# Kernel tuning notes

Hardware: AMD Instinct MI355X
Metric: run time of the kernel (lower is better)

Reference implementation:

```python
import jax, jax.numpy as jnp
import numpy as np

L, H, D, DH, F, V, S, B, CTX = 6, 12, 768, 64, 3072, 32000, 1024, 2, 1024
EPS = 1e-5


def layernorm(x, scale, bias):
    mu = jnp.mean(x, axis=-1, keepdims=True)
    var = jnp.mean(jnp.square(x - mu), axis=-1, keepdims=True)
    return (x - mu) * jax.lax.rsqrt(var + EPS) * scale + bias


def setup_inputs() -> dict:
    key = jax.random.key(0)
    ks = jax.random.split(key, 16)
    std = 0.02
    res_std = 0.02 * (2 * L) ** (-0.5)
    inp = {
        "X": jax.random.randint(ks[0], (B, S), 0, V),
        "emb": jax.random.normal(ks[1], (V, D), jnp.float32) * std,            # tied with head weight
        "pos_emb": jax.random.normal(ks[2], (CTX, D), jnp.float32) * 0.01,
        "Wq": jax.random.normal(ks[3], (L, H, D, DH), jnp.float32) * std,
        "bq": jnp.zeros((L, H, DH), jnp.float32),
        "Wk": jax.random.normal(ks[4], (L, H, D, DH), jnp.float32) * std,
        "bk": jnp.zeros((L, H, DH), jnp.float32),
        "Wv": jax.random.normal(ks[5], (L, H, D, DH), jnp.float32) * std,
        "bv": jnp.zeros((L, H, DH), jnp.float32),
        "Wo": jax.random.normal(ks[6], (L, H * DH, D), jnp.float32) * res_std,  # ResidualScaledLinear
        "bo": jnp.zeros((L, D), jnp.float32),
        "ln1_s": jnp.ones((L, D), jnp.float32),
        "ln1_b": jnp.zeros((L, D), jnp.float32),
        "ln2_s": jnp.ones((L, D), jnp.float32),
        "ln2_b": jnp.zeros((L, D), jnp.float32),
        "W1": jax.random.normal(ks[7], (L, D, F), jnp.float32) * std,
        "b1": jnp.zeros((L, F), jnp.float32),
        "W2": jax.random.normal(ks[8], (L, F, D), jnp.float32) * res_std,       # ResidualScaledLinear
        "b2": jnp.zeros((L, D), jnp.float32),
        "lnf_s": jnp.ones((D,), jnp.float32),
        "lnf_b": jnp.zeros((D,), jnp.float32),
        "head_b": jnp.zeros((V,), jnp.float32),
    }
    return inp


def decoder_forward(X, emb, pos_emb, Wq, bq, Wk, bk, Wv, bv, Wo, bo,
                    ln1_s, ln1_b, ln2_s, ln2_b, W1, b1, W2, b2,
                    lnf_s, lnf_b, head_b):
    seq = X.shape[1]
    x = emb[X] + pos_emb[:seq]                      # [B,S,D]
    causal = jnp.tril(jnp.ones((seq, seq), bool))   # tril mask buffer
    scale = 1.0 / jnp.sqrt(jnp.float32(DH))
    for l in range(L):
        xn = layernorm(x, ln1_s[l], ln1_b[l])
        q = jnp.einsum('bsd,hdk->bhsk', xn, Wq[l]) + bq[l][None, :, None, :]
        k = jnp.einsum('bsd,hdk->bhsk', xn, Wk[l]) + bk[l][None, :, None, :]
        v = jnp.einsum('bsd,hdk->bhsk', xn, Wv[l]) + bv[l][None, :, None, :]
        scores = jnp.einsum('bhsk,bhtk->bhst', q, k) * scale
        scores = jnp.where(causal, scores, -jnp.inf)
        attn = jax.nn.softmax(scores, axis=-1)
        out = jnp.einsum('bhst,bhtk->bshk', attn, v).reshape(x.shape[0], seq, H * DH)
        x = x + out @ Wo[l] + bo[l]
        xn2 = layernorm(x, ln2_s[l], ln2_b[l])
        x = x + jax.nn.relu(xn2 @ W1[l] + b1[l]) @ W2[l] + b2[l]
    x = layernorm(x, lnf_s, lnf_b)
    return x @ emb.T + head_b                       # tied head weight


def reference(X, emb, pos_emb, Wq, bq, Wk, bk, Wv, bv, Wo, bo,
              ln1_s, ln1_b, ln2_s, ln2_b, W1, b1, W2, b2,
              lnf_s, lnf_b, head_b):
    return decoder_forward(X, emb, pos_emb, Wq, bq, Wk, bk, Wv, bv, Wo, bo,
                           ln1_s, ln1_b, ln2_s, ln2_b, W1, b1, W2, b2,
                           lnf_s, lnf_b, head_b)
```

## Files before the change

kernel.cpp:

```cpp
#include <hip/hip_runtime.h>
#include <cstdint>
#include <cstddef>

#define CL 6
#define CH 12
#define CD 768
#define CDH 64
#define CF 3072
#define CV 32000
#define CS 1024
#define CB 2
#define CM (CB*CS)
#define CQS 2304
#define PSTRIDE 4224

typedef unsigned short u16;
typedef __bf16 bf16x8 __attribute__((ext_vector_type(8)));
typedef float f32x4 __attribute__((ext_vector_type(4)));

__device__ __forceinline__ float bf2f(u16 u) {
  union { unsigned int i; float f; } c; c.i = ((unsigned int)u) << 16; return c.f;
}
__device__ __forceinline__ u16 f2bf(float f) {
  union { float f; unsigned int i; } c; c.f = f;
  unsigned int lsb = (c.i >> 16) & 1u;
  c.i += 0x7fffu + lsb;
  return (u16)(c.i >> 16);
}

__device__ __forceinline__ void gload16(const u16* g, u16* l) {
  __builtin_amdgcn_global_load_lds(
      (const __attribute__((address_space(1))) void*)g,
      (__attribute__((address_space(3))) void*)l, 16, 0, 0);
}

__global__ __launch_bounds__(256) void convert_kernel(
    const float* __restrict__ src, u16* __restrict__ dst, int total)
{
  int idx = blockIdx.x * 256 + threadIdx.x;
  if (idx < total) dst[idx] = f2bf(src[idx]);
}

__global__ __launch_bounds__(256) void embed_kernel(
    const int* __restrict__ X, const float* __restrict__ emb,
    const float* __restrict__ pos, float* __restrict__ x)
{
  int idx = blockIdx.x * 256 + threadIdx.x;
  int m = idx / CD, d = idx - m * CD;
  int s = m & (CS - 1);
  x[idx] = emb[(size_t)X[m] * CD + d] + pos[s * CD + d];
}

__global__ __launch_bounds__(256) void ln_kernel(
    const float* __restrict__ x, const float* __restrict__ gs,
    const float* __restrict__ gb, u16* __restrict__ out)
{
  __shared__ float rs[4], rss[4];
  int row = blockIdx.x, tid = threadIdx.x;
  const float* xr = x + (size_t)row * CD;
  float a0 = xr[tid], a1 = xr[tid + 256], a2 = xr[tid + 512];
  float s = a0 + a1 + a2;
  float ss = a0 * a0 + a1 * a1 + a2 * a2;
#pragma unroll
  for (int sh = 32; sh > 0; sh >>= 1) {
    s  += __shfl_xor(s, sh, 64);
    ss += __shfl_xor(ss, sh, 64);
  }
  int w = tid >> 6;
  if ((tid & 63) == 0) { rs[w] = s; rss[w] = ss; }
  __syncthreads();
  s  = rs[0] + rs[1] + rs[2] + rs[3];
  ss = rss[0] + rss[1] + rss[2] + rss[3];
  float mu = s * (1.f / CD);
  float inv = rsqrtf(ss * (1.f / CD) - mu * mu + 1e-5f);
  u16* orow = out + (size_t)row * CD;
  orow[tid]       = f2bf((a0 - mu) * inv * gs[tid]       + gb[tid]);
  orow[tid + 256] = f2bf((a1 - mu) * inv * gs[tid + 256] + gb[tid + 256]);
  orow[tid + 512] = f2bf((a2 - mu) * inv * gs[tid + 512] + gb[tid + 512]);
}

__global__ __launch_bounds__(256) void trans_kernel(
    u16* __restrict__ dst, const float* __restrict__ src, int R, int C,
    int PB, long dstL)
{
  __shared__ float st[32][65];
  int r0 = blockIdx.x * 64, c0 = blockIdx.y * 32, bz = blockIdx.z;
  const float* s = src + (size_t)bz * R * C;
  u16* d = dst + (size_t)(bz / PB) * dstL + (size_t)(bz % PB) * R * C;
  int tx = threadIdx.x & 31, ty = threadIdx.x >> 5;
#pragma unroll
  for (int i = 0; i < 8; i++) {
    int r = ty + 8 * i;
    st[tx][r] = s[(size_t)(r0 + r) * C + c0 + tx];
  }
  __syncthreads();
  int j = threadIdx.x & 15, cbase = threadIdx.x >> 4;
#pragma unroll
  for (int i = 0; i < 2; i++) {
    int c = cbase + 16 * i;
    uint2 pk;
    u16* p = (u16*)&pk;
    p[0] = f2bf(st[c][4 * j + 0]);
    p[1] = f2bf(st[c][4 * j + 1]);
    p[2] = f2bf(st[c][4 * j + 2]);
    p[3] = f2bf(st[c][4 * j + 3]);
    *(uint2*)&d[(size_t)(c0 + c) * R + r0 + 4 * j] = pk;
  }
}

__global__ __launch_bounds__(256) void biaspack_kernel(
    const float* __restrict__ bq, const float* __restrict__ bk,
    const float* __restrict__ bv, float* __restrict__ dst)
{
  int idx = blockIdx.x * 256 + threadIdx.x;
  int l = idx / CQS, c = idx - l * CQS;
  float val;
  if (c < 768)       val = bq[l * 768 + c];
  else if (c < 1536) val = bk[l * 768 + c - 768];
  else               val = bv[l * 768 + c - 1536];
  dst[idx] = val;
}

template<bool RES, bool RELU, bool OUTBF>
__global__ __launch_bounds__(256) void gemm64v3_kernel(
    const u16* __restrict__ A, const u16* __restrict__ Bt,
    const float* __restrict__ bias, const float* __restrict__ res,
    void* __restrict__ outp, int M, int N, int K)
{
  __shared__ __align__(16) u16 As[64 * 32];
  __shared__ __align__(16) u16 Bs[64 * 32];
  int tid = threadIdx.x;
  int m0 = blockIdx.y * 64, n0 = blockIdx.x * 64;
  int wv = tid >> 6, ln = tid & 63;
  int quad = ln >> 4, l16 = ln & 15;
  int wm = (wv >> 1) * 32, wn = (wv & 1) * 32;
  int srow = tid >> 2, scol = (tid & 3) * 8;
  const u16* gA = A  + (size_t)(m0 + srow) * K + scol;
  const u16* gB = Bt + (size_t)(n0 + srow) * K + scol;
  u16* lA = As + wv * 512;
  u16* lB = Bs + wv * 512;

  f32x4 acc[2][2];
  acc[0][0] = f32x4{0,0,0,0}; acc[0][1] = f32x4{0,0,0,0};
  acc[1][0] = f32x4{0,0,0,0}; acc[1][1] = f32x4{0,0,0,0};

  for (int kt = 0; kt < K; kt += 32) {
    __syncthreads();
    gload16(gA + kt, lA);
    gload16(gB + kt, lB);
    __syncthreads();
    bf16x8 af[2], bfr[2];
#pragma unroll
    for (int i = 0; i < 2; i++) {
      af[i]  = *reinterpret_cast<const bf16x8*>(&As[(wm + i * 16 + l16) * 32 + quad * 8]);
      bfr[i] = *reinterpret_cast<const bf16x8*>(&Bs[(wn + i * 16 + l16) * 32 + quad * 8]);
    }
#pragma unroll
    for (int i = 0; i < 2; i++)
#pragma unroll
      for (int j = 0; j < 2; j++)
        acc[i][j] = __builtin_amdgcn_mfma_f32_16x16x32_bf16(af[i], bfr[j], acc[i][j], 0, 0, 0);
  }

#pragma unroll
  for (int i = 0; i < 2; i++) {
    int gmb = m0 + wm + i * 16 + quad * 4;
#pragma unroll
    for (int j = 0; j < 2; j++) {
      int gn = n0 + wn + j * 16 + l16;
      float bsv = bias[gn];
#pragma unroll
      for (int rr = 0; rr < 4; rr++) {
        float val = acc[i][j][rr] + bsv;
        if (RELU) val = fmaxf(val, 0.f);
        size_t o = (size_t)(gmb + rr) * N + gn;
        if (RES) val += res[o];
        if (OUTBF) ((u16*)outp)[o] = f2bf(val);
        else       ((float*)outp)[o] = val;
      }
    }
  }
}

template<bool RES, bool RELU, bool OUTBF>
__global__ __launch_bounds__(256) void gemm128_kernel(
    const u16* __restrict__ A, const u16* __restrict__ Bt,
    const float* __restrict__ bias, const float* __restrict__ res,
    void* __restrict__ outp, int M, int N, int K)
{
  __shared__ __align__(16) u16 As[128 * 32];
  __shared__ __align__(16) u16 Bs[128 * 32];
  int tid = threadIdx.x;
  int nbm = M >> 7, nbn = N >> 7, nwg = nbm * nbn;
  int orig = blockIdx.x;
  int q8 = nwg >> 3, r8 = nwg & 7;
  int xcd = orig & 7;
  int t = ((xcd < r8) ? xcd * (q8 + 1) : r8 * (q8 + 1) + (xcd - r8) * q8) + (orig >> 3);
  int bm = t % nbm, bn = t / nbm;
  int m0 = bm << 7, n0 = bn << 7;

  int wv = tid >> 6, ln = tid & 63;
  int quad = ln >> 4, l16 = ln & 15;
  int wr = wv >> 1, wc = wv & 1;

  int srow = wv * 16 + (ln >> 2);
  int scol = (ln & 3) * 8;
  const u16* ga0 = A  + (size_t)(m0 + srow) * K + scol;
  const u16* ga1 = A  + (size_t)(m0 + srow + 64) * K + scol;
  const u16* gb0 = Bt + (size_t)(n0 + srow) * K + scol;
  const u16* gb1 = Bt + (size_t)(n0 + srow + 64) * K + scol;
  u16* lA0 = As + wv * 512;
  u16* lA1 = As + 2048 + wv * 512;
  u16* lB0 = Bs + wv * 512;
  u16* lB1 = Bs + 2048 + wv * 512;

  f32x4 acc[4][4];
#pragma unroll
  for (int i = 0; i < 4; i++)
#pragma unroll
    for (int j = 0; j < 4; j++) acc[i][j] = f32x4{0.f, 0.f, 0.f, 0.f};

  for (int kt = 0; kt < K; kt += 32) {
    __syncthreads();
    gload16(ga0 + kt, lA0);
    gload16(ga1 + kt, lA1);
    gload16(gb0 + kt, lB0);
    gload16(gb1 + kt, lB1);
    __syncthreads();
    bf16x8 af[4], bf[4];
#pragma unroll
    for (int i = 0; i < 4; i++)
      af[i] = *reinterpret_cast<const bf16x8*>(&As[(wr * 64 + i * 16 + l16) * 32 + quad * 8]);
#pragma unroll
    for (int j = 0; j < 4; j++)
      bf[j] = *reinterpret_cast<const bf16x8*>(&Bs[(wc * 64 + j * 16 + l16) * 32 + quad * 8]);
#pragma unroll
    for (int i = 0; i < 4; i++)
#pragma unroll
      for (int j = 0; j < 4; j++)
        acc[i][j] = __builtin_amdgcn_mfma_f32_16x16x32_bf16(af[i], bf[j], acc[i][j], 0, 0, 0);
  }

#pragma unroll
  for (int i = 0; i < 4; i++) {
    int gm = m0 + wr * 64 + i * 16 + quad * 4;
#pragma unroll
    for (int j = 0; j < 4; j++) {
      int gn = n0 + wc * 64 + j * 16 + l16;
      float bsv = bias[gn];
#pragma unroll
      for (int rr = 0; rr < 4; rr++) {
        float val = acc[i][j][rr] + bsv;
        if (RELU) val = fmaxf(val, 0.f);
        size_t oo = (size_t)(gm + rr) * N + gn;
        if (RES) val += res[oo];
        if (OUTBF) ((u16*)outp)[oo] = f2bf(val);
        else       ((float*)outp)[oo] = val;
      }
    }
  }
}

__global__ __launch_bounds__(256) void attn_mfma_kernel(
    const u16* __restrict__ qkv, u16* __restrict__ o, float* __restrict__ part)
{
  __shared__ __align__(16) u16 Ks[2][64 * 64];
  __shared__ __align__(16) u16 Vt[2][64 * 64];
  __shared__ __align__(16) u16 Ps[4 * 16 * 64];

  int tid = threadIdx.x;
  int a = blockIdx.x;
  int h = blockIdx.y, b = blockIdx.z;
  int wid = tid >> 6, lane = tid & 63, quad = lane >> 4, l16 = lane & 15;

  int qb, ts, te, chunk;
  if (a < 16) {
    qb = 15 - (a >> 1);
    int half = (qb + 1) >> 1;
    if (a & 1) { ts = 0; te = half - 1; chunk = 0; }
    else       { ts = half; te = qb;    chunk = 1; }
  } else { qb = 23 - a; ts = 0; te = qb; chunk = -1; }

  int q0 = qb * 64;
  size_t bh = (size_t)b * CS * CQS + h * CDH;

  const u16* kbase = qkv + bh + 768;
  const u16* vbase = qkv + bh + 1536;

  int t4 = (tid & 15) * 4, dg = (tid >> 4) * 4;

  bf16x8 aq[2];
  {
    const u16* qrow = qkv + bh + (size_t)(q0 + wid * 16 + l16) * CQS;
#pragma unroll
    for (int ks = 0; ks < 2; ks++) {
      uint4 t = *(const uint4*)(qrow + ks * 32 + quad * 8);
      aq[ks] = *reinterpret_cast<bf16x8*>(&t);
    }
  }

  f32x4 oacc[4];
  float mrow[4], lrow[4];
#pragma unroll
  for (int j = 0; j < 4; j++) oacc[j] = f32x4{0.f, 0.f, 0.f, 0.f};
#pragma unroll
  for (int r = 0; r < 4; r++) { mrow[r] = -1e30f; lrow[r] = 0.f; }

  {
    const u16* kb0 = kbase + (size_t)ts * 64 * CQS;
#pragma unroll
    for (int it = 0; it < 2; it++) {
      int c = it * 256 + tid;
      int row = c >> 3, c8l = c & 7;
      gload16(kb0 + (size_t)row * CQS + (((c8l ^ (row & 7)) * 8)),
              &Ks[0][(it * 256 + wid * 64) * 8]);
    }
    const u16* vb0 = vbase + (size_t)ts * 64 * CQS;
    uint2 vr[4];
#pragma unroll
    for (int i = 0; i < 4; i++)
      vr[i] = *(const uint2*)(vb0 + (size_t)(t4 + i) * CQS + dg);
#pragma unroll
    for (int j = 0; j < 4; j++) {
      int d = dg + j;
      uint2 pk;
      u16* p = (u16*)&pk;
      p[0] = ((const u16*)&vr[0])[j]; p[1] = ((const u16*)&vr[1])[j];
      p[2] = ((const u16*)&vr[2])[j]; p[3] = ((const u16*)&vr[3])[j];
      *(uint2*)&Vt[0][d * 64 + (((t4 >> 3) ^ (d & 7)) * 8) + (t4 & 4)] = pk;
    }
  }

  for (int tt = ts; tt <= te; tt++) {
    int t0 = tt * 64;
    int cur = (tt - ts) & 1;
    __syncthreads();
    bool hasnext = (tt < te);
    uint2 vr[4];
    if (hasnext) {
      const u16* vb2 = vbase + (size_t)(t0 + 64) * CQS;
#pragma unroll
      for (int i = 0; i < 4; i++)
        vr[i] = *(const uint2*)(vb2 + (size_t)(t4 + i) * CQS + dg);
      const u16* kb2 = kbase + (size_t)(t0 + 64) * CQS;
#pragma unroll
      for (int it = 0; it < 2; it++) {
        int c = it * 256 + tid;
        int row = c >> 3, c8l = c & 7;
        gload16(kb2 + (size_t)row * CQS + (((c8l ^ (row & 7)) * 8)),
                &Ks[cur ^ 1][(it * 256 + wid * 64) * 8]);
      }
    }

    f32x4 sacc[4];
#pragma unroll
    for (int j = 0; j < 4; j++) sacc[j] = f32x4{0.f, 0.f, 0.f, 0.f};
#pragma unroll
    for (int j = 0; j < 4; j++) {
      int row = j * 16 + l16;
#pragma unroll
      for (int ks = 0; ks < 2; ks++) {
        bf16x8 bk = *reinterpret_cast<const bf16x8*>(
            &Ks[cur][row * 64 + ((((ks * 4 + quad) ^ (row & 7)) * 8))]);
        sacc[j] = __builtin_amdgcn_mfma_f32_16x16x32_bf16(aq[ks], bk, sacc[j], 0, 0, 0);
      }
    }

    int qg0 = q0 + wid * 16 + quad * 4;
#pragma unroll
    for (int j = 0; j < 4; j++) {
      int tg = t0 + j * 16 + l16;
#pragma unroll
      for (int r = 0; r < 4; r++) {
        float s = sacc[j][r] * 0.125f;
        sacc[j][r] = (tg <= qg0 + r) ? s : -1e30f;
      }
    }

#pragma unroll
    for (int r = 0; r < 4; r++) {
      float m = fmaxf(fmaxf(sacc[0][r], sacc[1][r]), fmaxf(sacc[2][r], sacc[3][r]));
#pragma unroll
      for (int sh = 1; sh < 16; sh <<= 1) m = fmaxf(m, __shfl_xor(m, sh, 64));
      float mnew = fmaxf(mrow[r], m);
      float scal = __expf(mrow[r] - mnew);
      mrow[r] = mnew;
      lrow[r] *= scal;
#pragma unroll
      for (int j = 0; j < 4; j++) oacc[j][r] *= scal;
      float sum = 0.f;
#pragma unroll
      for (int j = 0; j < 4; j++) {
        float p = __expf(sacc[j][r] - mnew);
        sacc[j][r] = p;
        sum += p;
      }
#pragma unroll
      for (int sh = 1; sh < 16; sh <<= 1) sum += __shfl_xor(sum, sh, 64);
      lrow[r] += sum;
    }

    u16* Pw = Ps + wid * 1024;
#pragma unroll
    for (int j = 0; j < 4; j++) {
      int c = (l16 >> 3) + 2 * j;
#pragma unroll
      for (int r = 0; r < 4; r++) {
        int row = quad * 4 + r;
        Pw[row * 64 + (((c ^ (row & 7)) * 8) | (l16 & 7))] = f2bf(sacc[j][r]);
      }
    }

    bf16x8 ap[2];
#pragma unroll
    for (int ks = 0; ks < 2; ks++)
      ap[ks] = *reinterpret_cast<const bf16x8*>(
          &Pw[l16 * 64 + ((((ks * 4 + quad) ^ (l16 & 7)) * 8))]);
#pragma unroll
    for (int j = 0; j < 4; j++) {
      int row = j * 16 + l16;
#pragma unroll
      for (int ks = 0; ks < 2; ks++) {
        bf16x8 bv = *reinterpret_cast<const bf16x8*>(
            &Vt[cur][row * 64 + ((((ks * 4 + quad) ^ (row & 7)) * 8))]);
        oacc[j] = __builtin_amdgcn_mfma_f32_16x16x32_bf16(ap[ks], bv, oacc[j], 0, 0, 0);
      }
    }

    if (hasnext) {
#pragma unroll
      for (int j = 0; j < 4; j++) {
        int d = dg + j;
        uint2 pk;
        u16* p = (u16*)&pk;
        p[0] = ((const u16*)&vr[0])[j]; p[1] = ((const u16*)&vr[1])[j];
        p[2] = ((const u16*)&vr[2])[j]; p[3] = ((const u16*)&vr[3])[j];
        *(uint2*)&Vt[cur ^ 1][d * 64 + (((t4 >> 3) ^ (d & 7)) * 8) + (t4 & 4)] = pk;
      }
    }
  }

  if (chunk < 0) {
#pragma unroll
    for (int r = 0; r < 4; r++) {
      float inv = 1.f / lrow[r];
      int qg = q0 + wid * 16 + quad * 4 + r;
      u16* orow = o + (size_t)b * CS * CD + h * CDH + (size_t)qg * CD;
#pragma unroll
      for (int j = 0; j < 4; j++)
        orow[j * 16 + l16] = f2bf(oacc[j][r] * inv);
    }
  } else {
    float* Po = part + (size_t)(((b * CH + h) * 8 + (qb - 8)) * 2 + chunk) * PSTRIDE;
#pragma unroll
    for (int r = 0; r < 4; r++) {
      int row = wid * 16 + quad * 4 + r;
#pragma unroll
      for (int j = 0; j < 4; j++)
        Po[row * 64 + j * 16 + l16] = oacc[j][r];
      if (l16 == 0) { Po[4096 + row] = mrow[r]; Po[4160 + row] = lrow[r]; }
    }
  }
}

__global__ __launch_bounds__(256) void attn_combine_kernel(
    const float* __restrict__ part, u16* __restrict__ o)
{
  int qb = 8 + blockIdx.x, h = blockIdx.y, b = blockIdx.z;
  const float* P0 = part + (size_t)(((b * CH + h) * 8 + (qb - 8)) * 2) * PSTRIDE;
  const float* P1 = P0 + PSTRIDE;
  int t = threadIdx.x;
  int row = t >> 2, c0 = (t & 3) * 16;
  float m0 = P0[4096 + row], m1 = P1[4096 + row];
  float m = fmaxf(m0, m1);
  float w0 = __expf(m0 - m), w1 = __expf(m1 - m);
  float inv = 1.f / (P0[4160 + row] * w0 + P1[4160 + row] * w1);
  u16* orow = o + (size_t)b * CS * CD + h * CDH + (size_t)(qb * 64 + row) * CD;
#pragma unroll
  for (int j = 0; j < 16; j++) {
    int col = c0 + j;
    orow[col] = f2bf((P0[row * 64 + col] * w0 + P1[row * 64 + col] * w1) * inv);
  }
}

extern "C" void kernel_launch(void* const* d_in, const int* in_sizes, int n_in,
                              void* d_out, int out_size, void* d_ws, size_t ws_size,
                              hipStream_t stream) {
  const int*   X      = (const int*)d_in[0];
  const float* emb    = (const float*)d_in[1];
  const float* pos    = (const float*)d_in[2];
  const float* Wq     = (const float*)d_in[3];
  const float* bq     = (const float*)d_in[4];
  const float* Wk     = (const float*)d_in[5];
  const float* bk     = (const float*)d_in[6];
  const float* Wv     = (const float*)d_in[7];
  const float* bv     = (const float*)d_in[8];
  const float* Wo     = (const float*)d_in[9];
  const float* bo     = (const float*)d_in[10];
  const float* ln1s   = (const float*)d_in[11];
  const float* ln1b   = (const float*)d_in[12];
  const float* ln2s   = (const float*)d_in[13];
  const float* ln2b   = (const float*)d_in[14];
  const float* W1     = (const float*)d_in[15];
  const float* b1     = (const float*)d_in[16];
  const float* W2     = (const float*)d_in[17];
  const float* b2     = (const float*)d_in[18];
  const float* lnfs   = (const float*)d_in[19];
  const float* lnfb   = (const float*)d_in[20];
  const float* headb  = (const float*)d_in[21];
  (void)in_sizes; (void)n_in; (void)out_size;

  char* ws = (char*)d_ws;
  size_t off = 0;
  auto alloc = [&](size_t bytes) { void* p = ws + off; off += (bytes + 255) & ~(size_t)255; return p; };

  float* x     = (float*)alloc((size_t)CM * CD * 4);
  u16*   xn    = (u16*)  alloc((size_t)CM * CD * 2);
  u16*   qkvb  = (u16*)  alloc((size_t)CM * CQS * 2);
  u16*   ao    = (u16*)  alloc((size_t)CM * CD * 2);
  u16*   hb    = (u16*)  alloc((size_t)CM * CF * 2);
  u16*   embC  = (u16*)  alloc((size_t)CV * CD * 2);
  float* biasp = (float*)alloc((size_t)CL * CQS * 4);
  float* part  = (float*)alloc((size_t)CB * CH * 8 * 2 * PSTRIDE * 4);

  const size_t WQKV = (size_t)CQS * CD;
  const size_t WOO  = (size_t)CD * CD;
  const size_t WFF  = (size_t)CD * CF;
  size_t perLayerElems = WQKV + WOO + 2 * WFF;
  bool fused = (ws_size >= off + (size_t)CL * perLayerElems * 2 + 4096);
  int LW = fused ? CL : 1;
  u16* Wqkvt = (u16*)alloc((size_t)LW * WQKV * 2);
  u16* Wot   = (u16*)alloc((size_t)LW * WOO * 2);
  u16* W1t   = (u16*)alloc((size_t)LW * WFF * 2);
  u16* W2t   = (u16*)alloc((size_t)LW * WFF * 2);

  embed_kernel<<<CM * CD / 256, 256, 0, stream>>>(X, emb, pos, x);
  convert_kernel<<<(CV * CD) / 256, 256, 0, stream>>>(emb, embC, CV * CD);
  biaspack_kernel<<<(CL * CQS) / 256, 256, 0, stream>>>(bq, bk, bv, biasp);

  if (fused) {
    trans_kernel<<<dim3(CD / 64, CDH / 32, CL * CH), 256, 0, stream>>>(Wqkvt,              Wq, CD, CDH, CH, (long)WQKV);
    trans_kernel<<<dim3(CD / 64, CDH / 32, CL * CH), 256, 0, stream>>>(Wqkvt + 768 * 768,  Wk, CD, CDH, CH, (long)WQKV);
    trans_kernel<<<dim3(CD / 64, CDH / 32, CL * CH), 256, 0, stream>>>(Wqkvt + 1536 * 768, Wv, CD, CDH, CH, (long)WQKV);
    trans_kernel<<<dim3(CD / 64, CD / 32, CL), 256, 0, stream>>>(Wot, Wo, CD, CD, 1, (long)WOO);
    trans_kernel<<<dim3(CD / 64, CF / 32, CL), 256, 0, stream>>>(W1t, W1, CD, CF, 1, (long)WFF);
    trans_kernel<<<dim3(CF / 64, CD / 32, CL), 256, 0, stream>>>(W2t, W2, CF, CD, 1, (long)WFF);
  }

  const int QKV_TOT = CH * CD * CDH;

  for (int l = 0; l < CL; l++) {
    if (!fused) {
      trans_kernel<<<dim3(CD / 64, CDH / 32, CH), 256, 0, stream>>>(Wqkvt,              Wq + (size_t)l * QKV_TOT, CD, CDH, CH, (long)WQKV);
      trans_kernel<<<dim3(CD / 64, CDH / 32, CH), 256, 0, stream>>>(Wqkvt + 768 * 768,  Wk + (size_t)l * QKV_TOT, CD, CDH, CH, (long)WQKV);
      trans_kernel<<<dim3(CD / 64, CDH / 32, CH), 256, 0, stream>>>(Wqkvt + 1536 * 768, Wv + (size_t)l * QKV_TOT, CD, CDH, CH, (long)WQKV);
      trans_kernel<<<dim3(CD / 64, CD / 32, 1), 256, 0, stream>>>(Wot, Wo + (size_t)l * WOO, CD, CD, 1, (long)WOO);
      trans_kernel<<<dim3(CD / 64, CF / 32, 1), 256, 0, stream>>>(W1t, W1 + (size_t)l * WFF, CD, CF, 1, (long)WFF);
      trans_kernel<<<dim3(CF / 64, CD / 32, 1), 256, 0, stream>>>(W2t, W2 + (size_t)l * WFF, CF, CD, 1, (long)WFF);
    }
    int lw = fused ? l : 0;
    const u16* wqkv = Wqkvt + (size_t)lw * WQKV;
    const u16* wot  = Wot   + (size_t)lw * WOO;
    const u16* w1t  = W1t   + (size_t)lw * WFF;
    const u16* w2t  = W2t   + (size_t)lw * WFF;

    ln_kernel<<<CM, 256, 0, stream>>>(x, ln1s + l * CD, ln1b + l * CD, xn);

    gemm128_kernel<false, false, true><<<(CM / 128) * (CQS / 128), 256, 0, stream>>>(
        xn, wqkv, biasp + l * CQS, nullptr, qkvb, CM, CQS, CD);

    attn_mfma_kernel<<<dim3(24, CH, CB), 256, 0, stream>>>(qkvb, ao, part);
    attn_combine_kernel<<<dim3(8, CH, CB), 256, 0, stream>>>(part, ao);

    gemm64v3_kernel<true, false, false><<<dim3(CD / 64, CM / 64), 256, 0, stream>>>(
        ao, wot, bo + l * CD, x, x, CM, CD, CD);

    ln_kernel<<<CM, 256, 0, stream>>>(x, ln2s + l * CD, ln2b + l * CD, xn);

    gemm128_kernel<false, true, true><<<(CM / 128) * (CF / 128), 256, 0, stream>>>(
        xn, w1t, b1 + l * CF, nullptr, hb, CM, CF, CD);

    gemm64v3_kernel<true, false, false><<<dim3(CD / 64, CM / 64), 256, 0, stream>>>(
        hb, w2t, b2 + l * CD, x, x, CM, CD, CF);
  }

  ln_kernel<<<CM, 256, 0, stream>>>(x, lnfs, lnfb, xn);
  gemm128_kernel<false, false, false><<<(CM / 128) * (CV / 128), 256, 0, stream>>>(
      xn, embC, headb, nullptr, d_out, CM, CV, CD);
}
```

Baseline: 1.508 ms.

## Double-buffer GEMM tiles, add 256-tile head GEMM, lazy softmax rescale

Converts the 64- and 128-tile GEMM kernels to double-buffered shared memory, so the next K-slice is loaded while the current one runs on MFMA, with one barrier per iteration instead of two. Adds a new 256x256-tile, 512-thread GEMM with swizzled LDS for the large vocabulary head projection. In attention it raises wave priority around MFMA blocks and skips the online-softmax rescale unless the running max grows by more than a threshold. The lazy rescale trades exactness of the running max for fewer exp and multiply operations, and risks overflow if scores drift. Larger LDS use may lower occupancy.

```diff
diff --git a/kernel.cpp b/kernel.cpp
--- a/kernel.cpp
+++ b/kernel.cpp
@@ -127,8 +127,8 @@
     const float* __restrict__ bias, const float* __restrict__ res,
     void* __restrict__ outp, int M, int N, int K)
 {
-  __shared__ __align__(16) u16 As[64 * 32];
-  __shared__ __align__(16) u16 Bs[64 * 32];
+  __shared__ __align__(16) u16 As[2][64 * 32];
+  __shared__ __align__(16) u16 Bs[2][64 * 32];
   int tid = threadIdx.x;
   int m0 = blockIdx.y * 64, n0 = blockIdx.x * 64;
   int wv = tid >> 6, ln = tid & 63;
@@ -137,29 +137,33 @@
   int srow = tid >> 2, scol = (tid & 3) * 8;
   const u16* gA = A  + (size_t)(m0 + srow) * K + scol;
   const u16* gB = Bt + (size_t)(n0 + srow) * K + scol;
-  u16* lA = As + wv * 512;
-  u16* lB = Bs + wv * 512;
 
   f32x4 acc[2][2];
   acc[0][0] = f32x4{0,0,0,0}; acc[0][1] = f32x4{0,0,0,0};
   acc[1][0] = f32x4{0,0,0,0}; acc[1][1] = f32x4{0,0,0,0};
 
+  gload16(gA, &As[0][wv * 512]);
+  gload16(gB, &Bs[0][wv * 512]);
+  __syncthreads();
+  int cur = 0;
   for (int kt = 0; kt < K; kt += 32) {
-    __syncthreads();
-    gload16(gA + kt, lA);
-    gload16(gB + kt, lB);
-    __syncthreads();
+    if (kt + 32 < K) {
+      gload16(gA + kt + 32, &As[cur ^ 1][wv * 512]);
+      gload16(gB + kt + 32, &Bs[cur ^ 1][wv * 512]);
+    }
     bf16x8 af[2], bfr[2];
 #pragma unroll
     for (int i = 0; i < 2; i++) {
-      af[i]  = *reinterpret_cast<const bf16x8*>(&As[(wm + i * 16 + l16) * 32 + quad * 8]);
-      bfr[i] = *reinterpret_cast<const bf16x8*>(&Bs[(wn + i * 16 + l16) * 32 + quad * 8]);
+      af[i]  = *reinterpret_cast<const bf16x8*>(&As[cur][(wm + i * 16 + l16) * 32 + quad * 8]);
+      bfr[i] = *reinterpret_cast<const bf16x8*>(&Bs[cur][(wn + i * 16 + l16) * 32 + quad * 8]);
     }
 #pragma unroll
     for (int i = 0; i < 2; i++)
 #pragma unroll
       for (int j = 0; j < 2; j++)
         acc[i][j] = __builtin_amdgcn_mfma_f32_16x16x32_bf16(af[i], bfr[j], acc[i][j], 0, 0, 0);
+    __syncthreads();
+    cur ^= 1;
   }
 
 #pragma unroll
@@ -188,8 +192,8 @@
     const float* __restrict__ bias, const float* __restrict__ res,
     void* __restrict__ outp, int M, int N, int K)
 {
-  __shared__ __align__(16) u16 As[128 * 32];
-  __shared__ __align__(16) u16 Bs[128 * 32];
+  __shared__ __align__(16) u16 As[2][128 * 32];
+  __shared__ __align__(16) u16 Bs[2][128 * 32];
   int tid = threadIdx.x;
   int nbm = M >> 7, nbn = N >> 7, nwg = nbm * nbn;
   int orig = blockIdx.x;
@@ -209,10 +213,6 @@
   const u16* ga1 = A  + (size_t)(m0 + srow + 64) * K + scol;
   const u16* gb0 = Bt + (size_t)(n0 + srow) * K + scol;
   const u16* gb1 = Bt + (size_t)(n0 + srow + 64) * K + scol;
-  u16* lA0 = As + wv * 512;
-  u16* lA1 = As + 2048 + wv * 512;
-  u16* lB0 = Bs + wv * 512;
-  u16* lB1 = Bs + 2048 + wv * 512;
 
   f32x4 acc[4][4];
 #pragma unroll
@@ -220,25 +220,33 @@
 #pragma unroll
     for (int j = 0; j < 4; j++) acc[i][j] = f32x4{0.f, 0.f, 0.f, 0.f};
 
+  gload16(ga0, &As[0][wv * 512]);
+  gload16(ga1, &As[0][2048 + wv * 512]);
+  gload16(gb0, &Bs[0][wv * 512]);
+  gload16(gb1, &Bs[0][2048 + wv * 512]);
+  __syncthreads();
+  int cur = 0;
   for (int kt = 0; kt < K; kt += 32) {
-    __syncthreads();
-    gload16(ga0 + kt, lA0);
-    gload16(ga1 + kt, lA1);
-    gload16(gb0 + kt, lB0);
-    gload16(gb1 + kt, lB1);
-    __syncthreads();
+    if (kt + 32 < K) {
+      gload16(ga0 + kt + 32, &As[cur ^ 1][wv * 512]);
+      gload16(ga1 + kt + 32, &As[cur ^ 1][2048 + wv * 512]);
+      gload16(gb0 + kt + 32, &Bs[cur ^ 1][wv * 512]);
+      gload16(gb1 + kt + 32, &Bs[cur ^ 1][2048 + wv * 512]);
+    }
     bf16x8 af[4], bf[4];
 #pragma unroll
     for (int i = 0; i < 4; i++)
-      af[i] = *reinterpret_cast<const bf16x8*>(&As[(wr * 64 + i * 16 + l16) * 32 + quad * 8]);
+      af[i] = *reinterpret_cast<const bf16x8*>(&As[cur][(wr * 64 + i * 16 + l16) * 32 + quad * 8]);
 #pragma unroll
     for (int j = 0; j < 4; j++)
-      bf[j] = *reinterpret_cast<const bf16x8*>(&Bs[(wc * 64 + j * 16 + l16) * 32 + quad * 8]);
+      bf[j] = *reinterpret_cast<const bf16x8*>(&Bs[cur][(wc * 64 + j * 16 + l16) * 32 + quad * 8]);
 #pragma unroll
     for (int i = 0; i < 4; i++)
 #pragma unroll
       for (int j = 0; j < 4; j++)
         acc[i][j] = __builtin_amdgcn_mfma_f32_16x16x32_bf16(af[i], bf[j], acc[i][j], 0, 0, 0);
+    __syncthreads();
+    cur ^= 1;
   }
 
 #pragma unroll
@@ -254,6 +262,98 @@
         if (RELU) val = fmaxf(val, 0.f);
         size_t oo = (size_t)(gm + rr) * N + gn;
         if (RES) val += res[oo];
+        if (OUTBF) ((u16*)outp)[oo] = f2bf(val);
+        else       ((float*)outp)[oo] = val;
+      }
+    }
+  }
+}
+
+template<bool OUTBF>
+__global__ __launch_bounds__(512, 2) void gemm256_kernel(
+    const u16* __restrict__ A, const u16* __restrict__ Bt,
+    const float* __restrict__ bias, void* __restrict__ outp,
+    int M, int N, int K)
+{
+  __shared__ __align__(16) u16 As[2][256 * 64];
+  __shared__ __align__(16) u16 Bs[2][256 * 64];
+  int tid = threadIdx.x;
+  int nbm = M >> 8, nbn = N >> 8, nwg = nbm * nbn;
+  int orig = blockIdx.x;
+  int q8 = nwg >> 3, r8 = nwg & 7;
+  int xcd = orig & 7;
+  int t = ((xcd < r8) ? xcd * (q8 + 1) : r8 * (q8 + 1) + (xcd - r8) * q8) + (orig >> 3);
+  int bm = t % nbm, bn = t / nbm;
+  int m0 = bm << 8, n0 = bn << 8;
+
+  int wv = tid >> 6, ln = tid & 63;
+  int quad = ln >> 4, l16 = ln & 15;
+  int wr = wv >> 2, wc = wv & 3;
+
+  int srow = tid >> 3;
+  int scol = (((tid & 7) ^ (srow & 7)) * 8);
+  const u16* gA = A  + (size_t)(m0 + srow) * K + scol;
+  const u16* gB = Bt + (size_t)(n0 + srow) * K + scol;
+
+  f32x4 acc[8][4];
+#pragma unroll
+  for (int i = 0; i < 8; i++)
+#pragma unroll
+    for (int j = 0; j < 4; j++) acc[i][j] = f32x4{0.f, 0.f, 0.f, 0.f};
+
+  int nt = K >> 6;
+#pragma unroll
+  for (int it = 0; it < 4; it++) {
+    gload16(gA + (size_t)(it * 64) * K, &As[0][(it * 512 + wv * 64) * 8]);
+    gload16(gB + (size_t)(it * 64) * K, &Bs[0][(it * 512 + wv * 64) * 8]);
+  }
+  __syncthreads();
+  int cur = 0;
+  for (int tt = 0; tt < nt; tt++) {
+    if (tt + 1 < nt) {
+      int kt = (tt + 1) << 6;
+#pragma unroll
+      for (int it = 0; it < 4; it++) {
+        gload16(gA + (size_t)(it * 64) * K + kt, &As[cur ^ 1][(it * 512 + wv * 64) * 8]);
+        gload16(gB + (size_t)(it * 64) * K + kt, &Bs[cur ^ 1][(it * 512 + wv * 64) * 8]);
+      }
+    }
+    const u16* as = As[cur];
+    const u16* bs = Bs[cur];
+#pragma unroll
+    for (int h = 0; h < 2; h++) {
+      bf16x8 af[8], bf[4];
+#pragma unroll
+      for (int i = 0; i < 8; i++) {
+        int R = wr * 128 + i * 16 + l16;
+        af[i] = *reinterpret_cast<const bf16x8*>(&as[R * 64 + (((h * 4 + quad) ^ (R & 7)) * 8)]);
+      }
+#pragma unroll
+      for (int j = 0; j < 4; j++) {
+        int S = wc * 64 + j * 16 + l16;
+        bf[j] = *reinterpret_cast<const bf16x8*>(&bs[S * 64 + (((h * 4 + quad) ^ (S & 7)) * 8)]);
+      }
+#pragma unroll
+      for (int i = 0; i < 8; i++)
+#pragma unroll
+        for (int j = 0; j < 4; j++)
+          acc[i][j] = __builtin_amdgcn_mfma_f32_16x16x32_bf16(af[i], bf[j], acc[i][j], 0, 0, 0);
+    }
+    __syncthreads();
+    cur ^= 1;
+  }
+
+#pragma unroll
+  for (int i = 0; i < 8; i++) {
+    int gm = m0 + wr * 128 + i * 16 + quad * 4;
+#pragma unroll
+    for (int j = 0; j < 4; j++) {
+      int gn = n0 + wc * 64 + j * 16 + l16;
+      float bsv = bias[gn];
+#pragma unroll
+      for (int rr = 0; rr < 4; rr++) {
+        float val = acc[i][j][rr] + bsv;
+        size_t oo = (size_t)(gm + rr) * N + gn;
         if (OUTBF) ((u16*)outp)[oo] = f2bf(val);
         else       ((float*)outp)[oo] = val;
       }
@@ -355,6 +455,7 @@
     f32x4 sacc[4];
 #pragma unroll
     for (int j = 0; j < 4; j++) sacc[j] = f32x4{0.f, 0.f, 0.f, 0.f};
+    __builtin_amdgcn_s_setprio(1);
 #pragma unroll
     for (int j = 0; j < 4; j++) {
       int row = j * 16 + l16;
@@ -365,6 +466,7 @@
         sacc[j] = __builtin_amdgcn_mfma_f32_16x16x32_bf16(aq[ks], bk, sacc[j], 0, 0, 0);
       }
     }
+    __builtin_amdgcn_s_setprio(0);
 
     int qg0 = q0 + wid * 16 + quad * 4;
 #pragma unroll
@@ -377,21 +479,33 @@
       }
     }
 
+    float tmax[4];
 #pragma unroll
     for (int r = 0; r < 4; r++) {
       float m = fmaxf(fmaxf(sacc[0][r], sacc[1][r]), fmaxf(sacc[2][r], sacc[3][r]));
 #pragma unroll
       for (int sh = 1; sh < 16; sh <<= 1) m = fmaxf(m, __shfl_xor(m, sh, 64));
-      float mnew = fmaxf(mrow[r], m);
-      float scal = __expf(mrow[r] - mnew);
-      mrow[r] = mnew;
-      lrow[r] *= scal;
-#pragma unroll
-      for (int j = 0; j < 4; j++) oacc[j][r] *= scal;
+      tmax[r] = m;
+    }
+    bool grow = (tmax[0] > mrow[0] + 8.f) || (tmax[1] > mrow[1] + 8.f) ||
+                (tmax[2] > mrow[2] + 8.f) || (tmax[3] > mrow[3] + 8.f);
+    if (__any(grow)) {
+#pragma unroll
+      for (int r = 0; r < 4; r++) {
+        float mnew = fmaxf(mrow[r], tmax[r]);
+        float scal = __expf(mrow[r] - mnew);
+        mrow[r] = mnew;
+        lrow[r] *= scal;
+#pragma unroll
+        for (int j = 0; j < 4; j++) oacc[j][r] *= scal;
+      }
+    }
+#pragma unroll
+    for (int r = 0; r < 4; r++) {
       float sum = 0.f;
 #pragma unroll
       for (int j = 0; j < 4; j++) {
-        float p = __expf(sacc[j][r] - mnew);
+        float p = __expf(sacc[j][r] - mrow[r]);
         sacc[j][r] = p;
         sum += p;
       }
@@ -416,6 +530,7 @@
     for (int ks = 0; ks < 2; ks++)
       ap[ks] = *reinterpret_cast<const bf16x8*>(
           &Pw[l16 * 64 + ((((ks * 4 + quad) ^ (l16 & 7)) * 8))]);
+    __builtin_amdgcn_s_setprio(1);
 #pragma unroll
     for (int j = 0; j < 4; j++) {
       int row = j * 16 + l16;
@@ -426,6 +541,7 @@
         oacc[j] = __builtin_amdgcn_mfma_f32_16x16x32_bf16(ap[ks], bv, oacc[j], 0, 0, 0);
       }
     }
+    __builtin_amdgcn_s_setprio(0);
 
     if (hasnext) {
 #pragma unroll
@@ -585,6 +701,6 @@
   }
 
   ln_kernel<<<CM, 256, 0, stream>>>(x, lnfs, lnfb, xn);
-  gemm128_kernel<false, false, false><<<(CM / 128) * (CV / 128), 256, 0, stream>>>(
-      xn, embC, headb, nullptr, d_out, CM, CV, CD);
-}
+  gemm256_kernel<false><<<(CM / 256) * (CV / 256), 512, 0, stream>>>(
+      xn, embC, headb, d_out, CM, CV, CD);
+}
```

Measured after the change: 1.476 ms. -2.1%, faster.
